# Kernel tuning notes

Hardware: AMD Instinct MI355X
Metric: run time of the kernel (lower is better)

Reference implementation:

```python
import jax, jax.numpy as jnp
import numpy as np

N_NODES = 10000
N_EDGES = 160000
HID = 128
N_LAYERS = 6
N_RBF = 50
CUTOFF = 10.0
EDGE_IN = 2 * HID + N_RBF + 1  # 307


def setup_inputs() -> dict:
    key = jax.random.key(0)
    ks = jax.random.split(key, 24)
    s = 0.05
    inp = {
        'atomic_numbers': jax.random.randint(ks[0], (N_NODES,), 0, 100),
        'coords': jax.random.normal(ks[1], (N_NODES, 3), jnp.float32),
        'edge_index': jax.random.randint(ks[2], (2, N_EDGES), 0, N_NODES),
        'embed': jax.random.normal(ks[3], (100, HID), jnp.float32) * s,
        # message_net (stacked over layers)
        'mw1': jax.random.normal(ks[4], (N_LAYERS, EDGE_IN, HID), jnp.float32) * s,
        'mb1': jnp.zeros((N_LAYERS, HID), jnp.float32),
        'mw2': jax.random.normal(ks[5], (N_LAYERS, HID, HID), jnp.float32) * s,
        'mb2': jnp.zeros((N_LAYERS, HID), jnp.float32),
        # coord_net
        'cw1': jax.random.normal(ks[6], (N_LAYERS, HID, HID), jnp.float32) * s,
        'cb1': jnp.zeros((N_LAYERS, HID), jnp.float32),
        'cw2': jax.random.normal(ks[7], (N_LAYERS, HID, 1), jnp.float32) * s,
        'cb2': jnp.zeros((N_LAYERS, 1), jnp.float32),
        # feature_net
        'fw': jax.random.normal(ks[8], (N_LAYERS, 2 * HID, HID), jnp.float32) * s,
        'fb': jnp.zeros((N_LAYERS, HID), jnp.float32),
        # energy_predictor
        'ew1': jax.random.normal(ks[9], (HID, HID), jnp.float32) * s,
        'eb1': jnp.zeros((HID,), jnp.float32),
        'ew2': jax.random.normal(ks[10], (HID, 1), jnp.float32) * s,
        'eb2': jnp.zeros((1,), jnp.float32),
    }
    return inp


def _forward(atomic_numbers, coords, edge_index, embed,
             mw1, mb1, mw2, mb2, cw1, cb1, cw2, cb2, fw, fb,
             ew1, eb1, ew2, eb2):
    silu = jax.nn.silu
    n = coords.shape[0]
    row, col = edge_index[0], edge_index[1]
    feats = embed[atomic_numbers]                    # [N, H]
    # RBF edge attributes (computed once from initial coords)
    d = jnp.linalg.norm(coords[row] - coords[col], axis=-1)[:, None]  # [E,1]
    centers = jnp.linspace(0.0, CUTOFF, N_RBF)
    width = CUTOFF / N_RBF
    rbf = jnp.exp(-((d - centers) ** 2) / width)
    cut = 0.5 * (jnp.cos(jnp.pi * d / CUTOFF) + 1.0) * (d < CUTOFF).astype(d.dtype)
    edge_attr = rbf * cut                            # [E, 50]
    for l in range(N_LAYERS):
        diff = coords[row] - coords[col]             # [E, 3]
        edist = jnp.sum(diff * diff, axis=-1, keepdims=True)  # squared dist, [E,1]
        ef = jnp.concatenate([feats[row], feats[col], edist, edge_attr], axis=-1)
        m = silu(silu(ef @ mw1[l] + mb1[l]) @ mw2[l] + mb2[l])        # [E, H]
        w = silu(m @ cw1[l] + cb1[l]) @ cw2[l] + cb2[l]               # [E, 1]
        coords = coords.at[row].add(w * diff)                         # equivariant coord update
        agg = jax.ops.segment_sum(m, row, num_segments=n)             # [N, H]
        feats = silu(jnp.concatenate([feats, agg], axis=-1) @ fw[l] + fb[l])
    atom_e = silu(feats @ ew1 + eb1) @ ew2 + eb2     # [N, 1]
    return jnp.sum(atom_e)


def reference(atomic_numbers, coords, edge_index, embed,
              mw1, mb1, mw2, mb2, cw1, cb1, cw2, cb2, fw, fb,
              ew1, eb1, ew2, eb2):
    return _forward(atomic_numbers, coords, edge_index, embed,
                    mw1, mb1, mw2, mb2, cw1, cb1, cw2, cb2, fw, fb,
                    ew1, eb1, ew2, eb2)
```

## Files before the change

### kernel.cpp

```cpp
#include <hip/hip_runtime.h>
#include <hip/hip_bf16.h>
#include <math.h>

#define N_NODES  10000
#define N_EDGES  160000
#define HID      128
#define N_LAYERS 6
#define N_RBF    50
#define EDGE_IN  307
#define M_TILE   64
#define N_TILES  (N_EDGES / M_TILE)

typedef short bf16x8 __attribute__((ext_vector_type(8)));
typedef float f32x4  __attribute__((ext_vector_type(4)));

__device__ __forceinline__ float silu_f(float x) {
    float e = __expf(-x);
    return x * __builtin_amdgcn_rcpf(1.0f + e);
}
__device__ __forceinline__ short f2bf(float f) {
    union { float f; unsigned u; } v; v.f = f;
    unsigned r = v.u + 0x7FFFu + ((v.u >> 16) & 1u);
    return (short)(r >> 16);
}
__device__ __forceinline__ float bf2f(unsigned short s) {
    union { float f; unsigned u; } v; v.u = ((unsigned)s) << 16;
    return v.f;
}
__device__ __forceinline__ unsigned pk_bf(float a, float b) {
    __hip_bfloat162 h = __float22bfloat162_rn(float2{a, b});
    unsigned u; __builtin_memcpy(&u, &h, 4); return u;
}


__global__ void init_feats_kernel(const int* __restrict__ an,
                                  const float* __restrict__ embed,
                                  short* __restrict__ featsB) {
    int idx = blockIdx.x * blockDim.x + threadIdx.x;
    if (idx < N_NODES * HID) {
        int i = idx >> 7, j = idx & 127;
        featsB[idx] = f2bf(embed[an[i] * HID + j]);
    }
}

__global__ void hist_kernel(const int* __restrict__ row, int* __restrict__ cnt) {
    int e = blockIdx.x * blockDim.x + threadIdx.x;
    if (e < N_EDGES) atomicAdd(&cnt[row[e]], 1);
}

__global__ void scan_kernel(const int* __restrict__ cnt, int* __restrict__ cursor) {
    __shared__ int buf[256];
    __shared__ int carry;
    int tid = threadIdx.x;
    if (tid == 0) carry = 0;
    __syncthreads();
    for (int base = 0; base < N_NODES; base += 256) {
        int v = (base + tid < N_NODES) ? cnt[base + tid] : 0;
        buf[tid] = v;
        __syncthreads();
        for (int off = 1; off < 256; off <<= 1) {
            int x = (tid >= off) ? buf[tid - off] : 0;
            __syncthreads();
            buf[tid] += x;
            __syncthreads();
        }
        int excl = buf[tid] - v + carry;
        if (base + tid < N_NODES) cursor[base + tid] = excl;
        int tot = buf[255];
        __syncthreads();
        if (tid == 0) carry += tot;
        __syncthreads();
    }
}

__global__ void scatter_kernel(const int* __restrict__ row, int* __restrict__ cursor,
                               int* __restrict__ sorted) {
    int e = blockIdx.x * blockDim.x + threadIdx.x;
    if (e < N_EDGES) {
        int p = atomicAdd(&cursor[row[e]], 1);
        sorted[p] = e;
    }
}

__global__ void edgegeom_kernel(const int* __restrict__ sorted,
                                const int* __restrict__ erow, const int* __restrict__ ecol,
                                const float* __restrict__ coords,
                                float* __restrict__ d0, float* __restrict__ cut0) {
    int p = blockIdx.x * 256 + threadIdx.x;
    if (p < N_EDGES) {
        int e = sorted[p];
        int r = erow[e], c = ecol[e];
        float dx = coords[3*r]   - coords[3*c];
        float dy = coords[3*r+1] - coords[3*c+1];
        float dz = coords[3*r+2] - coords[3*c+2];
        float d = sqrtf(dx*dx + dy*dy + dz*dz);
        d0[p] = d;
        cut0[p] = (d < 10.0f) ? 0.5f * (__cosf(0.31415926535f * d) + 1.0f) : 0.0f;
    }
}

#define SZ_M1E 8192
#define SZ_P   32768
#define SZ_M2  16384
#define SZ_C1  16384
#define SZ_F   32768
#define WT_L   (SZ_M1E + SZ_P + SZ_M2 + SZ_C1 + SZ_F)
__global__ void wtrans_kernel(const float* __restrict__ mw1, const float* __restrict__ mw2,
                              const float* __restrict__ cw1, const float* __restrict__ fw,
                              short* __restrict__ wtm1e, short* __restrict__ wtp,
                              short* __restrict__ wtm2, short* __restrict__ wtc1,
                              short* __restrict__ wtf) {
    int idx = blockIdx.x * blockDim.x + threadIdx.x;
    if (idx >= N_LAYERS * WT_L) return;
    int l = idx / WT_L;
    int r = idx - l * WT_L;
    const float* m1 = mw1 + (size_t)l * EDGE_IN * HID;
    if (r < SZ_M1E) {
        int n = r >> 6, k = r & 63;
        float v = 0.f;
        if (k == 0) v = m1[(size_t)256 * HID + n];
        else if (k <= 50) v = m1[(size_t)(256 + k) * HID + n];
        wtm1e[(size_t)l * SZ_M1E + r] = f2bf(v);
    } else if ((r -= SZ_M1E) < SZ_P) {
        int n = r >> 7, k = r & 127;
        float v = (n < HID) ? m1[(size_t)k * HID + n]
                            : m1[(size_t)(HID + k) * HID + (n - HID)];
        wtp[(size_t)l * SZ_P + r] = f2bf(v);
    } else if ((r -= SZ_P) < SZ_M2) {
        int n = r >> 7, k = r & 127;
        wtm2[(size_t)l * SZ_M2 + r] = f2bf(mw2[(size_t)l * HID * HID + (size_t)k * HID + n]);
    } else if ((r -= SZ_M2) < SZ_C1) {
        int n = r >> 7, k = r & 127;
        wtc1[(size_t)l * SZ_C1 + r] = f2bf(cw1[(size_t)l * HID * HID + (size_t)k * HID + n]);
    } else {
        r -= SZ_C1;
        int n = r >> 8, k = r & 255;
        wtf[(size_t)l * SZ_F + r] = f2bf(fw[(size_t)l * 2 * HID * HID + (size_t)k * HID + n]);
    }
}

__global__ __launch_bounds__(256) void p_kernel(
    const short* __restrict__ featsB, const short* __restrict__ wtp,
    short* __restrict__ Pg)
{
    __shared__ short sA[32][136];
    const int tid = threadIdx.x;
    const int n0 = blockIdx.x * 32;
    const int wave = tid >> 6, lane = tid & 63, quad = lane >> 4, lm = lane & 15;

    {
        int el = tid >> 3, kq = (tid & 7) * 16;
        int node = n0 + el;
        if (node < N_NODES) {
            const bf16x8* src = (const bf16x8*)&featsB[(size_t)node * HID + kq];
            *(bf16x8*)&sA[el][kq]     = src[0];
            *(bf16x8*)&sA[el][kq + 8] = src[1];
        } else {
            *(bf16x8*)&sA[el][kq]     = (bf16x8)0;
            *(bf16x8*)&sA[el][kq + 8] = (bf16x8)0;
        }
    }
    bf16x8 bw[4][4];
    #pragma unroll
    for (int h = 0; h < 4; ++h)
        #pragma unroll
        for (int nb = 0; nb < 4; ++nb) {
            int col = wave * 64 + nb * 16 + lm;
            bw[h][nb] = *(const bf16x8*)&wtp[(size_t)col * HID + h * 32 + quad * 8];
        }
    __syncthreads();

    f32x4 acc[2][4];
    #pragma unroll
    for (int mt = 0; mt < 2; ++mt)
        #pragma unroll
        for (int nb = 0; nb < 4; ++nb) acc[mt][nb] = (f32x4)0.f;

    #pragma unroll
    for (int h = 0; h < 4; ++h) {
        bf16x8 af[2];
        af[0] = *(bf16x8*)&sA[lm][h * 32 + quad * 8];
        af[1] = *(bf16x8*)&sA[16 + lm][h * 32 + quad * 8];
        #pragma unroll
        for (int nb = 0; nb < 4; ++nb) {
            acc[0][nb] = __builtin_amdgcn_mfma_f32_16x16x32_bf16(af[0], bw[h][nb], acc[0][nb], 0, 0, 0);
            acc[1][nb] = __builtin_amdgcn_mfma_f32_16x16x32_bf16(af[1], bw[h][nb], acc[1][nb], 0, 0, 0);
        }
    }
    #pragma unroll
    for (int mt = 0; mt < 2; ++mt)
        #pragma unroll
        for (int r = 0; r < 4; ++r) {
            int node = n0 + mt * 16 + quad * 4 + r;
            if (node < N_NODES) {
                #pragma unroll
                for (int nb = 0; nb < 4; ++nb) {
                    int col = wave * 64 + nb * 16 + lm;
                    Pg[(size_t)node * 256 + col] = f2bf(acc[mt][nb][r]);
                }
            }
        }
}


__global__ __launch_bounds__(256) void edge_kernel(
    const int* __restrict__ sorted,
    const int* __restrict__ erow, const int* __restrict__ ecol,
    const float* __restrict__ coords, float* __restrict__ coords_next,
    const short* __restrict__ Pg,
    const float* __restrict__ d0g, const float* __restrict__ cut0g,
    const short* __restrict__ wtm1e, const float* __restrict__ mb1,
    const short* __restrict__ wtm2, const float* __restrict__ mb2,
    const short* __restrict__ wtc1, const float* __restrict__ cb1,
    const float* __restrict__ cw2, const float* __restrict__ cb2,
    float* __restrict__ agg)
{
    __shared__ short sH[M_TILE][136];
    __shared__ short sA[M_TILE][72];
    __shared__ int   srow[M_TILE];
    __shared__ int   scol[M_TILE];
    __shared__ float sdiff[M_TILE][3];
    __shared__ float sdist[M_TILE], sd0[M_TILE], scut[M_TILE], sW[M_TILE];
    __shared__ float sWp[M_TILE][4];
    __shared__ float sB1[HID], sB2[HID], sC1[HID], sV[HID];

    const int tid = threadIdx.x;
    const int p0 = blockIdx.x * M_TILE;
    const int wave = tid >> 6, lane = tid & 63, quad = lane >> 4, lm = lane & 15;
    const int colA = wave * 32 + lm, colB = colA + 16;

    if (tid < M_TILE) {
        int e = sorted[p0 + tid];
        int r = erow[e], c = ecol[e];
        srow[tid] = r; scol[tid] = c;
        float dx = coords[3*r]   - coords[3*c];
        float dy = coords[3*r+1] - coords[3*c+1];
        float dz = coords[3*r+2] - coords[3*c+2];
        sdiff[tid][0] = dx; sdiff[tid][1] = dy; sdiff[tid][2] = dz;
        sdist[tid] = dx*dx + dy*dy + dz*dz;
        sd0[tid]  = d0g[p0 + tid];
        scut[tid] = cut0g[p0 + tid];
    }
    if (tid < HID) {
        sB1[tid] = mb1[tid]; sB2[tid] = mb2[tid];
        sC1[tid] = cb1[tid]; sV[tid]  = cw2[tid];
    }
    const float cb2v = cb2[0];
    __syncthreads();

    {
        int el = tid >> 2, kq = (tid & 3) * 32;
        const short* p1 = &Pg[(size_t)srow[el] * 256 + kq];
        const short* p2 = &Pg[(size_t)scol[el] * 256 + 128 + kq];
        #pragma unroll
        for (int g = 0; g < 4; ++g) {
            bf16x8 a = *(const bf16x8*)&p1[g * 8];
            bf16x8 b = *(const bf16x8*)&p2[g * 8];
            bf16x8 o;
            #pragma unroll
            for (int j = 0; j < 8; j += 2) {
                float s0 = bf2f((unsigned short)a[j])     + bf2f((unsigned short)b[j]);
                float s1 = bf2f((unsigned short)a[j + 1]) + bf2f((unsigned short)b[j + 1]);
                unsigned u = pk_bf(s0, s1);
                o[j] = (short)(u & 0xFFFF); o[j + 1] = (short)(u >> 16);
            }
            *(bf16x8*)&sH[el][kq + g * 8] = o;
        }
    }
    {
        int el = tid >> 2, kq = (tid & 3) * 16;
        float dv = sd0[el], ct = scut[el], ds2 = sdist[el];
        #pragma unroll
        for (int g = 0; g < 2; ++g) {
            bf16x8 v;
            #pragma unroll
            for (int j = 0; j < 8; ++j) {
                int k = kq + g * 8 + j;
                float val = 0.f;
                if (k == 0) val = ds2;
                else if (k <= N_RBF) {
                    float cen = (float)(k - 1) * (10.0f / 49.0f);
                    float t = dv - cen;
                    val = __expf(-t * t * 5.0f) * ct;
                }
                v[j] = f2bf(val);
            }
            *(bf16x8*)&sA[el][kq + g * 8] = v;
        }
    }
    bf16x8 bw1[2][2];
    #pragma unroll
    for (int h = 0; h < 2; ++h) {
        bw1[h][0] = *(const bf16x8*)&wtm1e[(size_t)colA * 64 + h * 32 + quad * 8];
        bw1[h][1] = *(const bf16x8*)&wtm1e[(size_t)colB * 64 + h * 32 + quad * 8];
    }
    bf16x8 bw2[4][2];
    #pragma unroll
    for (int ks = 0; ks < 4; ++ks) {
        bw2[ks][0] = *(const bf16x8*)&wtm2[(size_t)colA * HID + ks * 32 + quad * 8];
        bw2[ks][1] = *(const bf16x8*)&wtm2[(size_t)colB * HID + ks * 32 + quad * 8];
    }
    __syncthreads();

    f32x4 acc[4][2];
    #pragma unroll
    for (int mt = 0; mt < 4; ++mt) { acc[mt][0] = (f32x4)0.f; acc[mt][1] = (f32x4)0.f; }

    #pragma unroll
    for (int h = 0; h < 2; ++h) {
        bf16x8 af[4];
        #pragma unroll
        for (int mt = 0; mt < 4; ++mt)
            af[mt] = *(bf16x8*)&sA[mt * 16 + lm][h * 32 + quad * 8];
        #pragma unroll
        for (int nb = 0; nb < 2; ++nb)
            #pragma unroll
            for (int mt = 0; mt < 4; ++mt)
                acc[mt][nb] = __builtin_amdgcn_mfma_f32_16x16x32_bf16(
                    af[mt], bw1[h][nb], acc[mt][nb], 0, 0, 0);
    }
    #pragma unroll
    for (int mt = 0; mt < 4; ++mt) {
        float bA = sB1[colA], bB = sB1[colB];
        #pragma unroll
        for (int r = 0; r < 4; ++r) {
            int row = mt * 16 + quad * 4 + r;
            float pA = bf2f((unsigned short)sH[row][colA]);
            float pB = bf2f((unsigned short)sH[row][colB]);
            float hA = silu_f(acc[mt][0][r] + pA + bA);
            float hB = silu_f(acc[mt][1][r] + pB + bB);
            unsigned u = pk_bf(hA, hB);
            sH[row][colA] = (short)(u & 0xFFFF);
            sH[row][colB] = (short)(u >> 16);
        }
        acc[mt][0] = (f32x4)0.f; acc[mt][1] = (f32x4)0.f;
    }
    __syncthreads();

    #pragma unroll
    for (int ks = 0; ks < 4; ++ks) {
        bf16x8 af[4];
        #pragma unroll
        for (int mt = 0; mt < 4; ++mt)
            af[mt] = *(bf16x8*)&sH[mt * 16 + lm][ks * 32 + quad * 8];
        #pragma unroll
        for (int nb = 0; nb < 2; ++nb)
            #pragma unroll
            for (int mt = 0; mt < 4; ++mt)
                acc[mt][nb] = __builtin_amdgcn_mfma_f32_16x16x32_bf16(
                    af[mt], bw2[ks][nb], acc[mt][nb], 0, 0, 0);
    }
    bf16x8 bw3[4][2];
    #pragma unroll
    for (int ks = 0; ks < 4; ++ks) {
        bw3[ks][0] = *(const bf16x8*)&wtc1[(size_t)colA * HID + ks * 32 + quad * 8];
        bw3[ks][1] = *(const bf16x8*)&wtc1[(size_t)colB * HID + ks * 32 + quad * 8];
    }
    __syncthreads();
    #pragma unroll
    for (int nb = 0; nb < 2; ++nb) {
        int col = wave * 32 + nb * 16 + lm;
        float b = sB2[col];
        #pragma unroll
        for (int mt = 0; mt < 4; ++mt) {
            float g = 0.f;
            #pragma unroll
            for (int r = 0; r < 4; ++r) {
                int row = mt * 16 + quad * 4 + r;
                float mv = silu_f(acc[mt][nb][r] + b);
                sH[row][col] = f2bf(mv);
                g += mv;
                if (r == 3 || srow[row + 1] != srow[row]) {
                    atomicAdd(&agg[(size_t)srow[row] * HID + col], g);
                    g = 0.f;
                }
            }
            acc[mt][nb] = (f32x4)0.f;
        }
    }
    __syncthreads();

    #pragma unroll
    for (int ks = 0; ks < 4; ++ks) {
        bf16x8 af[4];
        #pragma unroll
        for (int mt = 0; mt < 4; ++mt)
            af[mt] = *(bf16x8*)&sH[mt * 16 + lm][ks * 32 + quad * 8];
        #pragma unroll
        for (int nb = 0; nb < 2; ++nb)
            #pragma unroll
            for (int mt = 0; mt < 4; ++mt)
                acc[mt][nb] = __builtin_amdgcn_mfma_f32_16x16x32_bf16(
                    af[mt], bw3[ks][nb], acc[mt][nb], 0, 0, 0);
    }
    {
        float wp[4][4];
        #pragma unroll
        for (int mt = 0; mt < 4; ++mt)
            #pragma unroll
            for (int r = 0; r < 4; ++r) wp[mt][r] = 0.f;
        #pragma unroll
        for (int nb = 0; nb < 2; ++nb) {
            int col = wave * 32 + nb * 16 + lm;
            float b = sC1[col], vv = sV[col];
            #pragma unroll
            for (int mt = 0; mt < 4; ++mt)
                #pragma unroll
                for (int r = 0; r < 4; ++r)
                    wp[mt][r] += silu_f(acc[mt][nb][r] + b) * vv;
        }
        #pragma unroll
        for (int mt = 0; mt < 4; ++mt)
            #pragma unroll
            for (int r = 0; r < 4; ++r) {
                float v = wp[mt][r];
                v += __shfl_xor(v, 1); v += __shfl_xor(v, 2);
                v += __shfl_xor(v, 4); v += __shfl_xor(v, 8);
                if (lm == 0) sWp[mt * 16 + quad * 4 + r][wave] = v;
            }
    }
    __syncthreads();
    if (tid < M_TILE)
        sW[tid] = cb2v + sWp[tid][0] + sWp[tid][1] + sWp[tid][2] + sWp[tid][3];
    __syncthreads();
    if (tid < M_TILE) {
        bool leader = (tid == 0) || (srow[tid] != srow[tid - 1]);
        if (leader) {
            int rr = srow[tid];
            float ax = 0.f, ay = 0.f, az = 0.f;
            for (int k = tid; k < M_TILE && srow[k] == rr; ++k) {
                ax += sW[k] * sdiff[k][0];
                ay += sW[k] * sdiff[k][1];
                az += sW[k] * sdiff[k][2];
            }
            atomicAdd(&coords_next[3*rr+0], ax);
            atomicAdd(&coords_next[3*rr+1], ay);
            atomicAdd(&coords_next[3*rr+2], az);
        }
    }
}

__global__ __launch_bounds__(256) void node_kernel(
    const short* __restrict__ featsB, const float* __restrict__ agg,
    const short* __restrict__ wtf, const float* __restrict__ fb,
    short* __restrict__ outB)
{
    __shared__ short sA[32][72];
    __shared__ short sO[32][136];
    __shared__ float sFb[HID];

    const int tid = threadIdx.x;
    const int n0 = blockIdx.x * 32;
    const int wave = tid >> 6, lane = tid & 63, quad = lane >> 4, lm = lane & 15;

    if (tid < HID) sFb[tid] = fb[tid];

    f32x4 acc[2][2];
    acc[0][0] = (f32x4)0.f; acc[0][1] = (f32x4)0.f;
    acc[1][0] = (f32x4)0.f; acc[1][1] = (f32x4)0.f;
    __syncthreads();

    for (int c = 0; c < 4; ++c) {
        int k0 = c * 64;
        bf16x8 bw[2][2];
        #pragma unroll
        for (int h = 0; h < 2; ++h) {
            int col0 = wave * 32 + lm;
            bw[h][0] = *(const bf16x8*)&wtf[(size_t)col0 * 256 + k0 + h * 32 + quad * 8];
            bw[h][1] = *(const bf16x8*)&wtf[(size_t)(col0 + 16) * 256 + k0 + h * 32 + quad * 8];
        }
        {
            int el = tid >> 3, kq = (tid & 7) * 8;
            int node = n0 + el;
            if (node < N_NODES) {
                if (c < 2) {
                    *(bf16x8*)&sA[el][kq] =
                        *(const bf16x8*)&featsB[(size_t)node * HID + k0 + kq];
                } else {
                    const float* ap = &agg[(size_t)node * HID + (k0 - 128) + kq];
                    bf16x8 v;
                    #pragma unroll
                    for (int j = 0; j < 8; j += 2) {
                        unsigned u = pk_bf(ap[j], ap[j + 1]);
                        v[j] = (short)(u & 0xFFFF); v[j + 1] = (short)(u >> 16);
                    }
                    *(bf16x8*)&sA[el][kq] = v;
                }
            } else {
                *(bf16x8*)&sA[el][kq] = (bf16x8)0;
            }
        }
        __syncthreads();
        #pragma unroll
        for (int h = 0; h < 2; ++h) {
            bf16x8 af[2];
            af[0] = *(bf16x8*)&sA[lm][h * 32 + quad * 8];
            af[1] = *(bf16x8*)&sA[16 + lm][h * 32 + quad * 8];
            #pragma unroll
            for (int nb = 0; nb < 2; ++nb) {
                acc[0][nb] = __builtin_amdgcn_mfma_f32_16x16x32_bf16(af[0], bw[h][nb], acc[0][nb], 0, 0, 0);
                acc[1][nb] = __builtin_amdgcn_mfma_f32_16x16x32_bf16(af[1], bw[h][nb], acc[1][nb], 0, 0, 0);
            }
        }
        __syncthreads();
    }
    #pragma unroll
    for (int mt = 0; mt < 2; ++mt) {
        float bA = sFb[wave * 32 + lm], bB = sFb[wave * 32 + 16 + lm];
        #pragma unroll
        for (int r = 0; r < 4; ++r) {
            int row = mt * 16 + quad * 4 + r;
            float hA = silu_f(acc[mt][0][r] + bA);
            float hB = silu_f(acc[mt][1][r] + bB);
            unsigned u = pk_bf(hA, hB);
            sO[row][wave * 32 + lm]      = (short)(u & 0xFFFF);
            sO[row][wave * 32 + 16 + lm] = (short)(u >> 16);
        }
    }
    __syncthreads();
    {
        int row = tid >> 3, ch = (tid & 7) * 8;
        int node = n0 + row;
        if (node < N_NODES) {
            *(bf16x8*)&outB[(size_t)node * HID + ch]      = *(bf16x8*)&sO[row][ch];
            *(bf16x8*)&outB[(size_t)node * HID + 64 + ch] = *(bf16x8*)&sO[row][64 + ch];
        }
    }
}

#define FMA8(r, aq) \
    acc[r][0] += (aq)*b0.x; acc[r][1] += (aq)*b0.y; acc[r][2] += (aq)*b0.z; acc[r][3] += (aq)*b0.w; \
    acc[r][4] += (aq)*b1.x; acc[r][5] += (aq)*b1.y; acc[r][6] += (aq)*b1.z; acc[r][7] += (aq)*b1.w;

__global__ __launch_bounds__(256) void energy_kernel(
    const short* __restrict__ featsB,
    const float* __restrict__ ew1, const float* __restrict__ eb1,
    const float* __restrict__ ew2, const float* __restrict__ eb2,
    float* __restrict__ out)
{
    __shared__ float sA[64][20];
    __shared__ float sB[16][HID];
    __shared__ float sV[HID];
    __shared__ float red[256];
    int tid = threadIdx.x;
    int n0 = blockIdx.x * 64;
    const int tr = tid >> 4, tc = tid & 15;
    const int r0 = tr * 4, c0 = tc * 4, c1 = c0 + 64;
    const int el = tid >> 2, kq = (tid & 3) * 4;

    if (tid < HID) sV[tid] = ew2[tid];

    float acc[4][8];
    #pragma unroll
    for (int i = 0; i < 4; i++)
        #pragma unroll
        for (int j = 0; j < 8; j++) acc[i][j] = 0.f;

    for (int kt = 0; kt < 8; ++kt) {
        int k0 = kt * 16;
        {
            int k = k0 + kq;
            int node = n0 + el;
            float4 v = make_float4(0,0,0,0);
            if (node < N_NODES) {
                const unsigned short* p = (const unsigned short*)&featsB[(size_t)node * HID + k];
                v.x = bf2f(p[0]); v.y = bf2f(p[1]); v.z = bf2f(p[2]); v.w = bf2f(p[3]);
            }
            *(float4*)&sA[el][kq] = v;
        }
        {
            int bk = tid >> 4, bj = (tid & 15) * 8;
            int k = k0 + bk;
            *(float4*)&sB[bk][bj]     = *(const float4*)&ew1[(size_t)k * HID + bj];
            *(float4*)&sB[bk][bj + 4] = *(const float4*)&ew1[(size_t)k * HID + bj + 4];
        }
        __syncthreads();
        #pragma unroll
        for (int kk4 = 0; kk4 < 4; ++kk4) {
            float4 a0 = *(const float4*)&sA[r0 + 0][kk4 * 4];
            float4 a1 = *(const float4*)&sA[r0 + 1][kk4 * 4];
            float4 a2 = *(const float4*)&sA[r0 + 2][kk4 * 4];
            float4 a3 = *(const float4*)&sA[r0 + 3][kk4 * 4];
            #pragma unroll
            for (int q = 0; q < 4; ++q) {
                int kk = kk4 * 4 + q;
                float4 b0 = *(const float4*)&sB[kk][c0];
                float4 b1 = *(const float4*)&sB[kk][c1];
                float q0 = ((const float*)&a0)[q], q1 = ((const float*)&a1)[q];
                float q2 = ((const float*)&a2)[q], q3 = ((const float*)&a3)[q];
                FMA8(0, q0) FMA8(1, q1) FMA8(2, q2) FMA8(3, q3)
            }
        }
        __syncthreads();
    }
    float part = 0.f;
    #pragma unroll
    for (int i = 0; i < 4; i++) {
        int node = n0 + r0 + i;
        if (node < N_NODES) {
            #pragma unroll
            for (int j = 0; j < 4; j++) {
                part += silu_f(acc[i][j]     + eb1[c0+j]) * sV[c0+j];
                part += silu_f(acc[i][4 + j] + eb1[c1+j]) * sV[c1+j];
            }
        }
    }
    red[tid] = part;
    __syncthreads();
    for (int s = 128; s > 0; s >>= 1) {
        if (tid < s) red[tid] += red[tid + s];
        __syncthreads();
    }
    if (tid == 0) {
        float v = red[0];
        if (blockIdx.x == 0) v += eb2[0] * (float)N_NODES;
        atomicAdd(out, v);
    }
}


extern "C" void kernel_launch(void* const* d_in, const int* in_sizes, int n_in,
                              void* d_out, int out_size, void* d_ws, size_t ws_size,
                              hipStream_t stream)
{
    const int*   an     = (const int*)  d_in[0];
    const float* coords = (const float*)d_in[1];
    const int*   ei     = (const int*)  d_in[2];
    const float* embed  = (const float*)d_in[3];
    const float* mw1 = (const float*)d_in[4];
    const float* mb1 = (const float*)d_in[5];
    const float* mw2 = (const float*)d_in[6];
    const float* mb2 = (const float*)d_in[7];
    const float* cw1 = (const float*)d_in[8];
    const float* cb1 = (const float*)d_in[9];
    const float* cw2 = (const float*)d_in[10];
    const float* cb2 = (const float*)d_in[11];
    const float* fw  = (const float*)d_in[12];
    const float* fb  = (const float*)d_in[13];
    const float* ew1 = (const float*)d_in[14];
    const float* eb1 = (const float*)d_in[15];
    const float* ew2 = (const float*)d_in[16];
    const float* eb2 = (const float*)d_in[17];
    float* out = (float*)d_out;

    char* w = (char*)d_ws;
    size_t off = 0;
    auto alloc = [&](size_t bytes) -> char* {
        char* p = w + off;
        off = (off + bytes + 511) & ~(size_t)511;
        return p;
    };
    short* featsB0 = (short*)alloc((size_t)N_NODES * HID * 2);
    short* featsB1 = (short*)alloc((size_t)N_NODES * HID * 2);
    short* Pg      = (short*)alloc((size_t)N_NODES * 256 * 2);
    float* agg     = (float*)alloc((size_t)N_NODES * HID * 4);
    float* cA      = (float*)alloc((size_t)N_NODES * 3 * 4);
    float* cB      = (float*)alloc((size_t)N_NODES * 3 * 4);
    float* d0      = (float*)alloc((size_t)N_EDGES * 4);
    float* cut0    = (float*)alloc((size_t)N_EDGES * 4);
    int*   sorted  = (int*)  alloc((size_t)N_EDGES * 4);
    int*   cnt     = (int*)  alloc((size_t)N_NODES * 4);
    int*   cursor  = (int*)  alloc((size_t)N_NODES * 4);
    short* wtm1e   = (short*)alloc((size_t)N_LAYERS * SZ_M1E * 2);
    short* wtp     = (short*)alloc((size_t)N_LAYERS * SZ_P * 2);
    short* wtm2    = (short*)alloc((size_t)N_LAYERS * SZ_M2 * 2);
    short* wtc1    = (short*)alloc((size_t)N_LAYERS * SZ_C1 * 2);
    short* wtf     = (short*)alloc((size_t)N_LAYERS * SZ_F * 2);

    const int* erow = ei;
    const int* ecol = ei + N_EDGES;

    hipMemsetAsync(cnt, 0, (size_t)N_NODES * 4, stream);
    init_feats_kernel<<<(N_NODES * HID + 255) / 256, 256, 0, stream>>>(an, embed, featsB0);
    wtrans_kernel<<<(N_LAYERS * WT_L + 255) / 256, 256, 0, stream>>>(
        mw1, mw2, cw1, fw, wtm1e, wtp, wtm2, wtc1, wtf);
    hipMemcpyAsync(cA, coords, (size_t)N_NODES * 3 * 4, hipMemcpyDeviceToDevice, stream);
    hist_kernel<<<(N_EDGES + 255) / 256, 256, 0, stream>>>(erow, cnt);
    scan_kernel<<<1, 256, 0, stream>>>(cnt, cursor);
    scatter_kernel<<<(N_EDGES + 255) / 256, 256, 0, stream>>>(erow, cursor, sorted);
    edgegeom_kernel<<<N_EDGES / 256, 256, 0, stream>>>(sorted, erow, ecol, cA, d0, cut0);
    p_kernel<<<(N_NODES + 31) / 32, 256, 0, stream>>>(featsB0, wtp, Pg);

    short* fc = featsB0; short* fn = featsB1;
    float* cc = cA;      float* cn = cB;
    for (int l = 0; l < N_LAYERS; ++l) {
        hipMemsetAsync(agg, 0, (size_t)N_NODES * HID * 4, stream);
        hipMemcpyAsync(cn, cc, (size_t)N_NODES * 3 * 4, hipMemcpyDeviceToDevice, stream);
        edge_kernel<<<N_TILES, 256, 0, stream>>>(
            sorted, erow, ecol, cc, cn, Pg, d0, cut0,
            wtm1e + (size_t)l * SZ_M1E, mb1 + (size_t)l * HID,
            wtm2  + (size_t)l * SZ_M2,  mb2 + (size_t)l * HID,
            wtc1  + (size_t)l * SZ_C1,  cb1 + (size_t)l * HID,
            cw2 + (size_t)l * HID,      cb2 + l, agg);
        node_kernel<<<(N_NODES + 31) / 32, 256, 0, stream>>>(
            fc, agg, wtf + (size_t)l * SZ_F, fb + (size_t)l * HID, fn);
        { short* t = fc; fc = fn; fn = t; }
        { float* t = cc; cc = cn; cn = t; }
        if (l + 1 < N_LAYERS)
            p_kernel<<<(N_NODES + 31) / 32, 256, 0, stream>>>(
                fc, wtp + (size_t)(l + 1) * SZ_P, Pg);
    }
    hipMemsetAsync(out, 0, 4, stream);
    energy_kernel<<<(N_NODES + 63) / 64, 256, 0, stream>>>(fc, ew1, eb1, ew2, eb2, out);
}
```

Before: 748.3 us.

## Fuse next-layer P projection, agg zeroing and coord copy into node kernel

The node kernel now computes the next layer's per-node P projection from its output tile, zeroes the aggregation buffer after reading it, and copies coordinates for the next layer. This removes the separate p_kernel, memset and memcpy launches each layer. The edge kernel also drops the shared-memory staging of biases and edge geometry in favour of per-thread registers and removes one barrier. The cost is redundant coordinate loads by four threads per edge and higher register pressure in the node kernel.

```diff
diff --git a/kernel.cpp b/kernel.cpp
--- a/kernel.cpp
+++ b/kernel.cpp
@@ -218,40 +218,36 @@
     __shared__ short sH[M_TILE][136];
     __shared__ short sA[M_TILE][72];
     __shared__ int   srow[M_TILE];
-    __shared__ int   scol[M_TILE];
     __shared__ float sdiff[M_TILE][3];
-    __shared__ float sdist[M_TILE], sd0[M_TILE], scut[M_TILE], sW[M_TILE];
+    __shared__ float sW[M_TILE];
     __shared__ float sWp[M_TILE][4];
-    __shared__ float sB1[HID], sB2[HID], sC1[HID], sV[HID];
 
     const int tid = threadIdx.x;
     const int p0 = blockIdx.x * M_TILE;
     const int wave = tid >> 6, lane = tid & 63, quad = lane >> 4, lm = lane & 15;
     const int colA = wave * 32 + lm, colB = colA + 16;
-
-    if (tid < M_TILE) {
-        int e = sorted[p0 + tid];
-        int r = erow[e], c = ecol[e];
-        srow[tid] = r; scol[tid] = c;
-        float dx = coords[3*r]   - coords[3*c];
-        float dy = coords[3*r+1] - coords[3*c+1];
-        float dz = coords[3*r+2] - coords[3*c+2];
-        sdiff[tid][0] = dx; sdiff[tid][1] = dy; sdiff[tid][2] = dz;
-        sdist[tid] = dx*dx + dy*dy + dz*dz;
-        sd0[tid]  = d0g[p0 + tid];
-        scut[tid] = cut0g[p0 + tid];
-    }
-    if (tid < HID) {
-        sB1[tid] = mb1[tid]; sB2[tid] = mb2[tid];
-        sC1[tid] = cb1[tid]; sV[tid]  = cw2[tid];
-    }
+    const int el = tid >> 2, sub = tid & 3;
+
+    int e = sorted[p0 + el];
+    int r = erow[e], c = ecol[e];
+    float dx = coords[3*r]   - coords[3*c];
+    float dy = coords[3*r+1] - coords[3*c+1];
+    float dz = coords[3*r+2] - coords[3*c+2];
+    float ds2 = dx*dx + dy*dy + dz*dz;
+    if (sub == 0) {
+        srow[el] = r;
+        sdiff[el][0] = dx; sdiff[el][1] = dy; sdiff[el][2] = dz;
+    }
+    float b1A = mb1[colA], b1B = mb1[colB];
+    float b2A = mb2[colA], b2B = mb2[colB];
+    float c1A = cb1[colA], c1B = cb1[colB];
+    float vA  = cw2[colA], vB  = cw2[colB];
     const float cb2v = cb2[0];
-    __syncthreads();
 
     {
-        int el = tid >> 2, kq = (tid & 3) * 32;
-        const short* p1 = &Pg[(size_t)srow[el] * 256 + kq];
-        const short* p2 = &Pg[(size_t)scol[el] * 256 + 128 + kq];
+        int kq = sub * 32;
+        const short* p1 = &Pg[(size_t)r * 256 + kq];
+        const short* p2 = &Pg[(size_t)c * 256 + 128 + kq];
         #pragma unroll
         for (int g = 0; g < 4; ++g) {
             bf16x8 a = *(const bf16x8*)&p1[g * 8];
@@ -268,8 +264,8 @@
         }
     }
     {
-        int el = tid >> 2, kq = (tid & 3) * 16;
-        float dv = sd0[el], ct = scut[el], ds2 = sdist[el];
+        float dv = d0g[p0 + el], ct = cut0g[p0 + el];
+        int kq = sub * 16;
         #pragma unroll
         for (int g = 0; g < 2; ++g) {
             bf16x8 v;
@@ -321,14 +317,13 @@
     }
     #pragma unroll
     for (int mt = 0; mt < 4; ++mt) {
-        float bA = sB1[colA], bB = sB1[colB];
-        #pragma unroll
-        for (int r = 0; r < 4; ++r) {
-            int row = mt * 16 + quad * 4 + r;
+        #pragma unroll
+        for (int r2 = 0; r2 < 4; ++r2) {
+            int row = mt * 16 + quad * 4 + r2;
             float pA = bf2f((unsigned short)sH[row][colA]);
             float pB = bf2f((unsigned short)sH[row][colB]);
-            float hA = silu_f(acc[mt][0][r] + pA + bA);
-            float hB = silu_f(acc[mt][1][r] + pB + bB);
+            float hA = silu_f(acc[mt][0][r2] + pA + b1A);
+            float hB = silu_f(acc[mt][1][r2] + pB + b1B);
             unsigned u = pk_bf(hA, hB);
             sH[row][colA] = (short)(u & 0xFFFF);
             sH[row][colB] = (short)(u >> 16);
@@ -360,17 +355,17 @@
     #pragma unroll
     for (int nb = 0; nb < 2; ++nb) {
         int col = wave * 32 + nb * 16 + lm;
-        float b = sB2[col];
+        float b = nb ? b2B : b2A;
         #pragma unroll
         for (int mt = 0; mt < 4; ++mt) {
             float g = 0.f;
             #pragma unroll
-            for (int r = 0; r < 4; ++r) {
-                int row = mt * 16 + quad * 4 + r;
-                float mv = silu_f(acc[mt][nb][r] + b);
+            for (int r2 = 0; r2 < 4; ++r2) {
+                int row = mt * 16 + quad * 4 + r2;
+                float mv = silu_f(acc[mt][nb][r2] + b);
                 sH[row][col] = f2bf(mv);
                 g += mv;
-                if (r == 3 || srow[row + 1] != srow[row]) {
+                if (r2 == 3 || srow[row + 1] != srow[row]) {
                     atomicAdd(&agg[(size_t)srow[row] * HID + col], g);
                     g = 0.f;
                 }
@@ -398,25 +393,25 @@
         #pragma unroll
         for (int mt = 0; mt < 4; ++mt)
             #pragma unroll
-            for (int r = 0; r < 4; ++r) wp[mt][r] = 0.f;
+            for (int r2 = 0; r2 < 4; ++r2) wp[mt][r2] = 0.f;
         #pragma unroll
         for (int nb = 0; nb < 2; ++nb) {
-            int col = wave * 32 + nb * 16 + lm;
-            float b = sC1[col], vv = sV[col];
+            float b = nb ? c1B : c1A;
+            float vv = nb ? vB : vA;
             #pragma unroll
             for (int mt = 0; mt < 4; ++mt)
                 #pragma unroll
-                for (int r = 0; r < 4; ++r)
-                    wp[mt][r] += silu_f(acc[mt][nb][r] + b) * vv;
+                for (int r2 = 0; r2 < 4; ++r2)
+                    wp[mt][r2] += silu_f(acc[mt][nb][r2] + b) * vv;
         }
         #pragma unroll
         for (int mt = 0; mt < 4; ++mt)
             #pragma unroll
-            for (int r = 0; r < 4; ++r) {
-                float v = wp[mt][r];
+            for (int r2 = 0; r2 < 4; ++r2) {
+                float v = wp[mt][r2];
                 v += __shfl_xor(v, 1); v += __shfl_xor(v, 2);
                 v += __shfl_xor(v, 4); v += __shfl_xor(v, 8);
-                if (lm == 0) sWp[mt * 16 + quad * 4 + r][wave] = v;
+                if (lm == 0) sWp[mt * 16 + quad * 4 + r2][wave] = v;
             }
     }
     __syncthreads();
@@ -441,24 +436,28 @@
 }
 
 __global__ __launch_bounds__(256) void node_kernel(
-    const short* __restrict__ featsB, const float* __restrict__ agg,
+    const short* __restrict__ featsB, float* __restrict__ agg,
     const short* __restrict__ wtf, const float* __restrict__ fb,
-    short* __restrict__ outB)
+    short* __restrict__ outB,
+    const short* __restrict__ wtp_next, short* __restrict__ Pg,
+    const float* __restrict__ csrc, float* __restrict__ cdst)
 {
     __shared__ short sA[32][72];
     __shared__ short sO[32][136];
-    __shared__ float sFb[HID];
 
     const int tid = threadIdx.x;
     const int n0 = blockIdx.x * 32;
     const int wave = tid >> 6, lane = tid & 63, quad = lane >> 4, lm = lane & 15;
 
-    if (tid < HID) sFb[tid] = fb[tid];
+    {
+        int idx = blockIdx.x * 256 + tid;
+        if (idx < 3 * N_NODES) cdst[idx] = csrc[idx];
+    }
+    float fbA = fb[wave * 32 + lm], fbB = fb[wave * 32 + 16 + lm];
 
     f32x4 acc[2][2];
     acc[0][0] = (f32x4)0.f; acc[0][1] = (f32x4)0.f;
     acc[1][0] = (f32x4)0.f; acc[1][1] = (f32x4)0.f;
-    __syncthreads();
 
     for (int c = 0; c < 4; ++c) {
         int k0 = c * 64;
@@ -477,7 +476,7 @@
                     *(bf16x8*)&sA[el][kq] =
                         *(const bf16x8*)&featsB[(size_t)node * HID + k0 + kq];
                 } else {
-                    const float* ap = &agg[(size_t)node * HID + (k0 - 128) + kq];
+                    float* ap = &agg[(size_t)node * HID + (k0 - 128) + kq];
                     bf16x8 v;
                     #pragma unroll
                     for (int j = 0; j < 8; j += 2) {
@@ -485,6 +484,8 @@
                         v[j] = (short)(u & 0xFFFF); v[j + 1] = (short)(u >> 16);
                     }
                     *(bf16x8*)&sA[el][kq] = v;
+                    *(float4*)&ap[0] = make_float4(0.f, 0.f, 0.f, 0.f);
+                    *(float4*)&ap[4] = make_float4(0.f, 0.f, 0.f, 0.f);
                 }
             } else {
                 *(bf16x8*)&sA[el][kq] = (bf16x8)0;
@@ -504,14 +505,23 @@
         }
         __syncthreads();
     }
+    bf16x8 bwp[4][4];
+    if (wtp_next) {
+        #pragma unroll
+        for (int ks = 0; ks < 4; ++ks)
+            #pragma unroll
+            for (int nb = 0; nb < 4; ++nb) {
+                int col = wave * 64 + nb * 16 + lm;
+                bwp[ks][nb] = *(const bf16x8*)&wtp_next[(size_t)col * HID + ks * 32 + quad * 8];
+            }
+    }
     #pragma unroll
     for (int mt = 0; mt < 2; ++mt) {
-        float bA = sFb[wave * 32 + lm], bB = sFb[wave * 32 + 16 + lm];
         #pragma unroll
         for (int r = 0; r < 4; ++r) {
             int row = mt * 16 + quad * 4 + r;
-            float hA = silu_f(acc[mt][0][r] + bA);
-            float hB = silu_f(acc[mt][1][r] + bB);
+            float hA = silu_f(acc[mt][0][r] + fbA);
+            float hB = silu_f(acc[mt][1][r] + fbB);
             unsigned u = pk_bf(hA, hB);
             sO[row][wave * 32 + lm]      = (short)(u & 0xFFFF);
             sO[row][wave * 32 + 16 + lm] = (short)(u >> 16);
@@ -525,6 +535,37 @@
             *(bf16x8*)&outB[(size_t)node * HID + ch]      = *(bf16x8*)&sO[row][ch];
             *(bf16x8*)&outB[(size_t)node * HID + 64 + ch] = *(bf16x8*)&sO[row][64 + ch];
         }
+    }
+    if (wtp_next) {
+        f32x4 ap2[2][4];
+        #pragma unroll
+        for (int mt = 0; mt < 2; ++mt)
+            #pragma unroll
+            for (int nb = 0; nb < 4; ++nb) ap2[mt][nb] = (f32x4)0.f;
+        #pragma unroll
+        for (int ks = 0; ks < 4; ++ks) {
+            bf16x8 af[2];
+            af[0] = *(bf16x8*)&sO[lm][ks * 32 + quad * 8];
+            af[1] = *(bf16x8*)&sO[16 + lm][ks * 32 + quad * 8];
+            #pragma unroll
+            for (int nb = 0; nb < 4; ++nb) {
+                ap2[0][nb] = __builtin_amdgcn_mfma_f32_16x16x32_bf16(af[0], bwp[ks][nb], ap2[0][nb], 0, 0, 0);
+                ap2[1][nb] = __builtin_amdgcn_mfma_f32_16x16x32_bf16(af[1], bwp[ks][nb], ap2[1][nb], 0, 0, 0);
+            }
+        }
+        #pragma unroll
+        for (int mt = 0; mt < 2; ++mt)
+            #pragma unroll
+            for (int r = 0; r < 4; ++r) {
+                int node = n0 + mt * 16 + quad * 4 + r;
+                if (node < N_NODES) {
+                    #pragma unroll
+                    for (int nb = 0; nb < 4; ++nb) {
+                        int col = wave * 64 + nb * 16 + lm;
+                        Pg[(size_t)node * 256 + col] = f2bf(ap2[mt][nb][r]);
+                    }
+                }
+            }
     }
 }
 
@@ -671,10 +712,12 @@
     const int* ecol = ei + N_EDGES;
 
     hipMemsetAsync(cnt, 0, (size_t)N_NODES * 4, stream);
+    hipMemsetAsync(agg, 0, (size_t)N_NODES * HID * 4, stream);
     init_feats_kernel<<<(N_NODES * HID + 255) / 256, 256, 0, stream>>>(an, embed, featsB0);
     wtrans_kernel<<<(N_LAYERS * WT_L + 255) / 256, 256, 0, stream>>>(
         mw1, mw2, cw1, fw, wtm1e, wtp, wtm2, wtc1, wtf);
     hipMemcpyAsync(cA, coords, (size_t)N_NODES * 3 * 4, hipMemcpyDeviceToDevice, stream);
+    hipMemcpyAsync(cB, coords, (size_t)N_NODES * 3 * 4, hipMemcpyDeviceToDevice, stream);
     hist_kernel<<<(N_EDGES + 255) / 256, 256, 0, stream>>>(erow, cnt);
     scan_kernel<<<1, 256, 0, stream>>>(cnt, cursor);
     scatter_kernel<<<(N_EDGES + 255) / 256, 256, 0, stream>>>(erow, cursor, sorted);
@@ -684,8 +727,6 @@
     short* fc = featsB0; short* fn = featsB1;
     float* cc = cA;      float* cn = cB;
     for (int l = 0; l < N_LAYERS; ++l) {
-        hipMemsetAsync(agg, 0, (size_t)N_NODES * HID * 4, stream);
-        hipMemcpyAsync(cn, cc, (size_t)N_NODES * 3 * 4, hipMemcpyDeviceToDevice, stream);
         edge_kernel<<<N_TILES, 256, 0, stream>>>(
             sorted, erow, ecol, cc, cn, Pg, d0, cut0,
             wtm1e + (size_t)l * SZ_M1E, mb1 + (size_t)l * HID,
@@ -693,12 +734,11 @@
             wtc1  + (size_t)l * SZ_C1,  cb1 + (size_t)l * HID,
             cw2 + (size_t)l * HID,      cb2 + l, agg);
         node_kernel<<<(N_NODES + 31) / 32, 256, 0, stream>>>(
-            fc, agg, wtf + (size_t)l * SZ_F, fb + (size_t)l * HID, fn);
+            fc, agg, wtf + (size_t)l * SZ_F, fb + (size_t)l * HID, fn,
+            (l + 1 < N_LAYERS) ? (wtp + (size_t)(l + 1) * SZ_P) : (const short*)nullptr,
+            Pg, cn, cc);
         { short* t = fc; fc = fn; fn = t; }
         { float* t = cc; cc = cn; cn = t; }
-        if (l + 1 < N_LAYERS)
-            p_kernel<<<(N_NODES + 31) / 32, 256, 0, stream>>>(
-                fc, wtp + (size_t)(l + 1) * SZ_P, Pg);
     }
     hipMemsetAsync(out, 0, 4, stream);
     energy_kernel<<<(N_NODES + 63) / 64, 256, 0, stream>>>(fc, ew1, eb1, ew2, eb2, out);
```

Result: faster. 711.4 us (-4.9%).
